# Kernel tuning notes

Measured on AMD Instinct MI355X. Metric: run time of the kernel, lower is better.

The kernel has to match this reference:

```python
import jax, jax.numpy as jnp
import numpy as np

D_MODEL = 1024
N_HEADS = 16
DEPTH = D_MODEL // N_HEADS


def setup_inputs() -> dict:
    key = jax.random.key(0)
    ks = jax.random.split(key, 11)
    B, S = 2, 2048
    s = 1.0 / np.sqrt(D_MODEL)
    return {
        "query": jax.random.normal(ks[0], (B, S, D_MODEL), jnp.float32),
        "key": jax.random.normal(ks[1], (B, S, D_MODEL), jnp.float32),
        "value": jax.random.normal(ks[2], (B, S, D_MODEL), jnp.float32),
        "Wq": jax.random.normal(ks[3], (D_MODEL, D_MODEL), jnp.float32) * s,
        "bq": jnp.zeros((D_MODEL,), jnp.float32),
        "Wk": jax.random.normal(ks[4], (D_MODEL, D_MODEL), jnp.float32) * s,
        "bk": jnp.zeros((D_MODEL,), jnp.float32),
        "Wv": jax.random.normal(ks[5], (D_MODEL, D_MODEL), jnp.float32) * s,
        "bv": jnp.zeros((D_MODEL,), jnp.float32),
        "Wo": jax.random.normal(ks[6], (D_MODEL, D_MODEL), jnp.float32) * s,
        "bo": jnp.zeros((D_MODEL,), jnp.float32),
    }


def _split_heads(x):
    B, S, _ = x.shape
    return x.reshape(B, S, N_HEADS, DEPTH).transpose(0, 2, 1, 3)  # [B,H,S,depth]


def reference(query, key, value, Wq, bq, Wk, bk, Wv, bv, Wo, bo):
    q = _split_heads(query @ Wq.T + bq)   # [B,H,S,d]
    k = _split_heads(key @ Wk.T + bk)
    v = _split_heads(value @ Wv.T + bv)
    scale = 1.0 / jnp.sqrt(jnp.asarray(DEPTH, jnp.float32))
    scores = jnp.einsum('bhqd,bhkd->bhqk', q, k) * scale  # [B,H,S,S]
    attn = jax.nn.softmax(scores, axis=-1)
    ctx = jnp.einsum('bhqk,bhkd->bhqd', attn, v)          # [B,H,S,d]
    B, H, S, d = ctx.shape
    ctx = ctx.transpose(0, 2, 1, 3).reshape(B, S, D_MODEL)
    out = ctx @ Wo.T + bo
    return out, attn
```

## Files before the change

### kernel.cpp

```cpp
#include <hip/hip_runtime.h>
#include <stdint.h>


#define DEV __device__ __forceinline__

typedef __attribute__((ext_vector_type(8))) short short8;
typedef __attribute__((ext_vector_type(4))) short short4v;
typedef __attribute__((ext_vector_type(4))) float f32x4;
typedef __attribute__((ext_vector_type(4))) uint32_t u32x4;

DEV short f2bf(float f) {
  uint32_t u = __builtin_bit_cast(uint32_t, f);
  u += 0x7fffu + ((u >> 16) & 1u);
  return (short)(u >> 16);
}

DEV uint32_t cvtpk_bf16(float a, float b) {
  uint32_t r;
  asm("v_cvt_pk_bf16_f32 %0, %1, %2" : "=v"(r) : "v"(a), "v"(b));
  return r;
}

DEV void gload_lds16(const void* g, void* l) {
  __builtin_amdgcn_global_load_lds(
      (const __attribute__((address_space(1))) void*)g,
      (__attribute__((address_space(3))) void*)l,
      16, 0, 0);
}

__global__ __launch_bounds__(256) void attn_fused(
    const short* __restrict__ q, const short* __restrict__ k,
    const short* __restrict__ vT, float* __restrict__ attn,
    short* __restrict__ ctx) {
  __shared__ __align__(16) char Ps[4 * 32 * 128];

  const int tid = threadIdx.x;
  const int lane = tid & 63;
  const int wm = tid >> 6;
  const int c = lane & 15;
  const int g = lane >> 4;
  const int orig = blockIdx.x;
  const int sid = (orig & 7) * 64 + (orig >> 3);
  const int qb = sid & 15;
  const int z = sid >> 4;

  const short* qz = q + (size_t)z * 131072 + (size_t)(qb * 128 + wm * 32) * 64;
  const short* kz = k + (size_t)z * 131072;
  const short* vz = vT + (size_t)z * 131072;
  float* az = attn + (size_t)z * 4194304 + (size_t)(qb * 128 + wm * 32) * 2048;

  short8 qf[2][2];
#pragma unroll
  for (int m = 0; m < 2; ++m)
#pragma unroll
    for (int kk = 0; kk < 2; ++kk)
      qf[m][kk] = *(const short8*)(qz + (m * 16 + c) * 64 + kk * 32 + g * 8);

  float l_part[2][4];
#pragma unroll
  for (int m = 0; m < 2; ++m)
#pragma unroll
    for (int j = 0; j < 4; ++j) l_part[m][j] = 0.f;

  for (int kt = 0; kt < 16; ++kt) {
    const short* kzt = kz + kt * 8192;
    f32x4 s[2][8];
#pragma unroll
    for (int m = 0; m < 2; ++m)
#pragma unroll
      for (int n = 0; n < 8; ++n) s[m][n] = f32x4{0.f, 0.f, 0.f, 0.f};
#pragma unroll
    for (int kk = 0; kk < 2; ++kk) {
#pragma unroll
      for (int n = 0; n < 8; ++n) {
        const short8 bf =
            *(const short8*)(kzt + (n * 16 + c) * 64 + kk * 32 + g * 8);
        s[0][n] = __builtin_amdgcn_mfma_f32_16x16x32_bf16(qf[0][kk], bf,
                                                          s[0][n], 0, 0, 0);
        s[1][n] = __builtin_amdgcn_mfma_f32_16x16x32_bf16(qf[1][kk], bf,
                                                          s[1][n], 0, 0, 0);
      }
    }
#pragma unroll
    for (int m = 0; m < 2; ++m)
#pragma unroll
      for (int j = 0; j < 4; ++j)
#pragma unroll
        for (int n = 0; n < 8; ++n) l_part[m][j] += __expf(s[m][n][j]);
  }

  float inv_l[2][4];
#pragma unroll
  for (int m = 0; m < 2; ++m)
#pragma unroll
    for (int j = 0; j < 4; ++j) {
      float l = l_part[m][j];
      l += __shfl_xor(l, 1, 64);
      l += __shfl_xor(l, 2, 64);
      l += __shfl_xor(l, 4, 64);
      l += __shfl_xor(l, 8, 64);
      inv_l[m][j] = 1.0f / l;
    }

  f32x4 o[2][4];
#pragma unroll
  for (int m = 0; m < 2; ++m)
#pragma unroll
    for (int n = 0; n < 4; ++n) o[m][n] = f32x4{0.f, 0.f, 0.f, 0.f};

  char* Pw = Ps + wm * 4096;

  for (int kt = 0; kt < 16; ++kt) {
    const short* kzt = kz + kt * 8192;
    f32x4 s[2][8];
#pragma unroll
    for (int m = 0; m < 2; ++m)
#pragma unroll
      for (int n = 0; n < 8; ++n) s[m][n] = f32x4{0.f, 0.f, 0.f, 0.f};
#pragma unroll
    for (int kk = 0; kk < 2; ++kk) {
#pragma unroll
      for (int n = 0; n < 8; ++n) {
        const short8 bf =
            *(const short8*)(kzt + (n * 16 + c) * 64 + kk * 32 + g * 8);
        s[0][n] = __builtin_amdgcn_mfma_f32_16x16x32_bf16(qf[0][kk], bf,
                                                          s[0][n], 0, 0, 0);
        s[1][n] = __builtin_amdgcn_mfma_f32_16x16x32_bf16(qf[1][kk], bf,
                                                          s[1][n], 0, 0, 0);
      }
    }
#pragma unroll
    for (int m = 0; m < 2; ++m)
#pragma unroll
      for (int j = 0; j < 4; ++j) {
        const float il = inv_l[m][j];
#pragma unroll
        for (int n = 0; n < 8; ++n) s[m][n][j] = __expf(s[m][n][j]) * il;
      }
#pragma unroll
    for (int m = 0; m < 2; ++m)
#pragma unroll
      for (int n = 0; n < 8; ++n)
#pragma unroll
        for (int j = 0; j < 4; ++j)
          __builtin_nontemporal_store(
              s[m][n][j], az + (size_t)(m * 16 + g * 4 + j) * 2048 +
                              kt * 128 + n * 16 + c);
#pragma unroll
    for (int kc = 0; kc < 4; ++kc) {
#pragma unroll
      for (int m = 0; m < 2; ++m)
#pragma unroll
        for (int nn = 0; nn < 2; ++nn)
#pragma unroll
          for (int j = 0; j < 4; ++j) {
            const int r = m * 16 + g * 4 + j;
            *(float*)(Pw + r * 128 +
                      (((nn * 16 + c) * 4) ^ ((r & 7) << 4))) =
                s[m][kc * 2 + nn][j];
          }
      short8 paf[2];
#pragma unroll
      for (int m = 0; m < 2; ++m) {
        const int r = m * 16 + c;
        const int X = (r & 7) << 4;
        const f32x4 lo = *(const f32x4*)(Pw + r * 128 + ((g * 32) ^ X));
        const f32x4 hi = *(const f32x4*)(Pw + r * 128 + ((g * 32 + 16) ^ X));
        u32x4 pk;
        pk[0] = cvtpk_bf16(lo[0], lo[1]);
        pk[1] = cvtpk_bf16(lo[2], lo[3]);
        pk[2] = cvtpk_bf16(hi[0], hi[1]);
        pk[3] = cvtpk_bf16(hi[2], hi[3]);
        paf[m] = __builtin_bit_cast(short8, pk);
      }
#pragma unroll
      for (int n2 = 0; n2 < 4; ++n2) {
        const short8 vf = *(const short8*)(vz + (size_t)(n2 * 16 + c) * 2048 +
                                           kt * 128 + kc * 32 + g * 8);
        o[0][n2] = __builtin_amdgcn_mfma_f32_16x16x32_bf16(paf[0], vf,
                                                           o[0][n2], 0, 0, 0);
        o[1][n2] = __builtin_amdgcn_mfma_f32_16x16x32_bf16(paf[1], vf,
                                                           o[1][n2], 0, 0, 0);
      }
    }
  }

  const int b = z >> 4, h = z & 15;
#pragma unroll
  for (int m = 0; m < 2; ++m)
#pragma unroll
    for (int n2 = 0; n2 < 4; ++n2)
#pragma unroll
      for (int j = 0; j < 4; ++j)
        ctx[((size_t)(b * 2048 + qb * 128 + wm * 32 + m * 16 + g * 4 + j)) *
                1024 + h * 64 + n2 * 16 + c] = f2bf(o[m][n2][j]);
}

enum { M_PROJ = 0, M_OUT = 3 };

struct GP {
  const void* A0; const void* A1; const void* A2;
  const short* B;
  const float* b0; const float* b1; const float* b2;
  void* C;
  int lda, ldb, K;
  long aBS, bBS;
};

template<int WM, int WN, int AM, int AN, bool CONVA, int MODE>
__global__ __launch_bounds__(256) void gemm_nt(GP p) {
  constexpr int BM = WM * 16 * AM;
  constexpr int BN = WN * 16 * AN;
  static_assert(WM * WN == 4, "4 waves / 256 threads");
  __shared__ __align__(16) char As[BM * 128];
  __shared__ __align__(16) char Bs[BN * 128];

  const int tid = threadIdx.x;
  const int lane = tid & 63;
  const int z = blockIdx.y;
  const int orig = blockIdx.x;
  const int sid = (orig & 7) * 32 + (orig >> 3);
  const int bm0 = (sid >> 3) * BM;
  const int bn0 = (sid & 7) * BN;

  const void* Aroot; const float* bias;
  if constexpr (MODE == M_PROJ) {
    if constexpr (CONVA)
      Aroot = (z == 0) ? p.A0 : (z == 1 ? p.A1 : p.A2);
    else
      Aroot = p.A0;
    bias = (z == 0) ? p.b0 : (z == 1 ? p.b1 : p.b2);
  } else {
    Aroot = p.A0; bias = p.b0;
  }

  f32x4 acc[AM][AN];
#pragma unroll
  for (int m = 0; m < AM; ++m)
#pragma unroll
    for (int n = 0; n < AN; ++n) acc[m][n] = f32x4{0.f, 0.f, 0.f, 0.f};

  const int wave = tid >> 6;
  const int wm = wave / WN;
  const int wn = wave % WN;

  const int nK = p.K >> 6;
  for (int kt = 0; kt < nK; ++kt) {
    if constexpr (CONVA) {
      const float* Af = (const float*)Aroot + (size_t)z * p.aBS +
                        (size_t)bm0 * p.lda + kt * 64;
#pragma unroll
      for (int sw = 0; sw < BM / 16; ++sw) {
        const int r = sw * 16 + (tid >> 4);
        const int s8 = tid & 15;
        const float4 v = *(const float4*)(Af + (size_t)r * p.lda + s8 * 4);
        short4v oo;
        oo[0] = f2bf(v.x); oo[1] = f2bf(v.y); oo[2] = f2bf(v.z); oo[3] = f2bf(v.w);
        const int boff = (r * 128 + s8 * 8) ^ ((r & 7) << 4);
        *(short4v*)(As + boff) = oo;
      }
    } else {
      const short* Ab = (const short*)Aroot + (size_t)z * p.aBS +
                        (size_t)bm0 * p.lda + kt * 64;
#pragma unroll
      for (int sw = 0; sw < BM / 32; ++sw) {
        const int r = sw * 32 + (tid >> 3);
        const int c8 = (tid & 7) ^ (r & 7);
        gload_lds16(Ab + (size_t)r * p.lda + c8 * 8, As + (sw * 256 + tid) * 16);
      }
    }
    {
      const short* Bb = p.B + (size_t)z * p.bBS + (size_t)bn0 * p.ldb + kt * 64;
#pragma unroll
      for (int sw = 0; sw < BN / 32; ++sw) {
        const int r = sw * 32 + (tid >> 3);
        const int c8 = (tid & 7) ^ (r & 7);
        gload_lds16(Bb + (size_t)r * p.ldb + c8 * 8, Bs + (sw * 256 + tid) * 16);
      }
    }
    __syncthreads();
#pragma unroll
    for (int kk = 0; kk < 2; ++kk) {
      const int kb = kk * 64 + (lane >> 4) * 16;
      short8 aF[AM], bF[AN];
#pragma unroll
      for (int m = 0; m < AM; ++m) {
        const int r = wm * (16 * AM) + m * 16 + (lane & 15);
        aF[m] = *(const short8*)(As + ((r * 128 + kb) ^ ((r & 7) << 4)));
      }
#pragma unroll
      for (int n = 0; n < AN; ++n) {
        const int r = wn * (16 * AN) + n * 16 + (lane & 15);
        bF[n] = *(const short8*)(Bs + ((r * 128 + kb) ^ ((r & 7) << 4)));
      }
#pragma unroll
      for (int m = 0; m < AM; ++m)
#pragma unroll
        for (int n = 0; n < AN; ++n)
          acc[m][n] = __builtin_amdgcn_mfma_f32_16x16x32_bf16(
              aF[m], bF[n], acc[m][n], 0, 0, 0);
    }
    __syncthreads();
  }

#pragma unroll
  for (int m = 0; m < AM; ++m) {
#pragma unroll
    for (int n = 0; n < AN; ++n) {
#pragma unroll
      for (int j = 0; j < 4; ++j) {
        const int gm = bm0 + wm * (16 * AM) + m * 16 + ((lane >> 4) << 2) + j;
        const int gn = bn0 + wn * (16 * AN) + n * 16 + (lane & 15);
        const float v = acc[m][n][j];
        if constexpr (MODE == M_PROJ) {
          float vb = v + bias[gn];
          if (z == 0) vb *= 0.125f;
          const int b = gm >> 11, s = gm & 2047;
          const int h = gn >> 6, d = gn & 63;
          short* C = (short*)p.C;
          if (z < 2) {
            C[(size_t)z * 4194304 + (((size_t)(b * 16 + h) * 2048 + s) * 64 + d)] = f2bf(vb);
          } else {
            C[(size_t)2 * 4194304 + (((size_t)(b * 16 + h) * 64 + d) * 2048 + s)] = f2bf(vb);
          }
        } else {
          __builtin_nontemporal_store(
              v + bias[gn], (float*)p.C + (size_t)gm * 1024 + gn);
        }
      }
    }
  }
}

__global__ __launch_bounds__(256) void cvt_all(
    const float* q, const float* k, const float* v, const float* w0,
    const float* w1, const float* w2, const float* w3, short* xb, short* Wb) {
  const int y = blockIdx.y;
  const float* src; short* dst; int n;
  if (y < 3) {
    src = (y == 0) ? q : (y == 1) ? k : v;
    dst = xb + (size_t)y * 4194304; n = 4194304;
  } else {
    src = (y == 3) ? w0 : (y == 4) ? w1 : (y == 5) ? w2 : w3;
    dst = Wb + (size_t)(y - 3) * 1048576; n = 1048576;
  }
  const int i = (blockIdx.x * 256 + threadIdx.x) * 4;
  if (i >= n) return;
  const float4 val = *(const float4*)(src + i);
  short4v s;
  s[0] = f2bf(val.x); s[1] = f2bf(val.y); s[2] = f2bf(val.z); s[3] = f2bf(val.w);
  *(short4v*)(dst + i) = s;
}

__global__ __launch_bounds__(256) void cvt_w(const float* w0, const float* w1,
                                             const float* w2, const float* w3,
                                             short* out) {
  const float* w = (blockIdx.y == 0) ? w0 : (blockIdx.y == 1) ? w1
                 : (blockIdx.y == 2) ? w2 : w3;
  short* o = out + (size_t)blockIdx.y * 1048576;
  const int i = (blockIdx.x * 256 + threadIdx.x) * 4;
  const float4 v = *(const float4*)(w + i);
  short4v s;
  s[0] = f2bf(v.x); s[1] = f2bf(v.y); s[2] = f2bf(v.z); s[3] = f2bf(v.w);
  *(short4v*)(o + i) = s;
}

extern "C" void kernel_launch(void* const* d_in, const int* in_sizes, int n_in,
                              void* d_out, int out_size, void* d_ws, size_t ws_size,
                              hipStream_t stream) {
  const float* query = (const float*)d_in[0];
  const float* key_  = (const float*)d_in[1];
  const float* value = (const float*)d_in[2];
  const float* Wq = (const float*)d_in[3];
  const float* bq = (const float*)d_in[4];
  const float* Wk = (const float*)d_in[5];
  const float* bk = (const float*)d_in[6];
  const float* Wv = (const float*)d_in[7];
  const float* bv = (const float*)d_in[8];
  const float* Wo = (const float*)d_in[9];
  const float* bo = (const float*)d_in[10];

  float* out  = (float*)d_out;
  float* attn = (float*)d_out + 4194304;
  short* ws   = (short*)d_ws;

  const bool big_ws = ws_size >= (size_t)64 * 1024 * 1024;

  if (big_ws) {
    short* xb  = ws;
    short* Wb  = ws + 3 * 4194304;
    short* qkv = ws + 3 * 4194304 + 4 * 1048576;
    short* ctx = qkv + 3 * 4194304;

    cvt_all<<<dim3(4096, 7), 256, 0, stream>>>(query, key_, value, Wq, Wk, Wv,
                                               Wo, xb, Wb);
    {
      GP p{};
      p.A0 = xb;
      p.B = Wb; p.b0 = bq; p.b1 = bk; p.b2 = bv;
      p.C = qkv;
      p.lda = 1024; p.ldb = 1024; p.K = 1024;
      p.aBS = 4194304; p.bBS = 1048576;
      gemm_nt<2, 2, 4, 4, false, M_PROJ><<<dim3(256, 3), 256, 0, stream>>>(p);
    }
    attn_fused<<<dim3(512), 256, 0, stream>>>(
        qkv, qkv + 4194304, qkv + 2 * 4194304, attn, ctx);
    {
      GP p{};
      p.A0 = ctx;
      p.B = Wb + 3 * 1048576;
      p.b0 = bo;
      p.C = out;
      p.lda = 1024; p.ldb = 1024; p.K = 1024;
      p.aBS = 0; p.bBS = 0;
      gemm_nt<2, 2, 4, 4, false, M_OUT><<<dim3(256, 1), 256, 0, stream>>>(p);
    }
  } else {
    short* Wb  = ws;
    short* qkv = ws + 4194304;
    short* ctx = ws + 4 * 4194304;

    cvt_w<<<dim3(1024, 4), 256, 0, stream>>>(Wq, Wk, Wv, Wo, Wb);
    {
      GP p{};
      p.A0 = query; p.A1 = key_; p.A2 = value;
      p.B = Wb; p.b0 = bq; p.b1 = bk; p.b2 = bv;
      p.C = qkv;
      p.lda = 1024; p.ldb = 1024; p.K = 1024;
      p.aBS = 0; p.bBS = 1048576;
      gemm_nt<2, 2, 4, 4, true, M_PROJ><<<dim3(256, 3), 256, 0, stream>>>(p);
    }
    attn_fused<<<dim3(512), 256, 0, stream>>>(
        qkv, qkv + 4194304, qkv + 2 * 4194304, attn, ctx);
    {
      GP p{};
      p.A0 = ctx;
      p.B = Wb + 3 * 1048576;
      p.b0 = bo;
      p.C = out;
      p.lda = 1024; p.ldb = 1024; p.K = 1024;
      p.aBS = 0; p.bBS = 0;
      gemm_nt<2, 2, 4, 4, false, M_OUT><<<dim3(256, 1), 256, 0, stream>>>(p);
    }
  }
}
```

Measured before the change: 302.9 us.

## Compute transposed scores so P feeds PV MFMA via shuffles instead of LDS

The attention kernel now computes S^T (K as the A operand, Q as B), so each lane holds four consecutive key columns. This allows vectorized 16-byte nontemporal stores of the attention matrix and lets the bf16 P fragment for the PV MFMA be assembled with cross-lane shuffles instead of an LDS round trip. Each wave now handles 16 query rows instead of 32, the grid doubles to 1024 blocks, and launch bounds request 4 blocks per CU. The cost is that K fragments are reused by half as many rows, so K and V global loads per unit of work double.

```diff
diff --git a/kernel.cpp b/kernel.cpp
--- a/kernel.cpp
+++ b/kernel.cpp
@@ -28,172 +28,124 @@
       16, 0, 0);
 }
 
-__global__ __launch_bounds__(256) void attn_fused(
+__global__ __launch_bounds__(256, 4) void attn_fused(
     const short* __restrict__ q, const short* __restrict__ k,
     const short* __restrict__ vT, float* __restrict__ attn,
     short* __restrict__ ctx) {
-  __shared__ __align__(16) char Ps[4 * 32 * 128];
-
   const int tid = threadIdx.x;
   const int lane = tid & 63;
   const int wm = tid >> 6;
   const int c = lane & 15;
   const int g = lane >> 4;
+  const bool godd = (g & 1) != 0;
+  const bool ghi = g >= 2;
   const int orig = blockIdx.x;
-  const int sid = (orig & 7) * 64 + (orig >> 3);
-  const int qb = sid & 15;
-  const int z = sid >> 4;
-
-  const short* qz = q + (size_t)z * 131072 + (size_t)(qb * 128 + wm * 32) * 64;
+  const int sid = (orig & 7) * 128 + (orig >> 3);
+  const int qb = sid & 31;
+  const int z = sid >> 5;
+
+  const short* qz = q + (size_t)z * 131072 + (size_t)(qb * 64 + wm * 16) * 64;
   const short* kz = k + (size_t)z * 131072;
   const short* vz = vT + (size_t)z * 131072;
-  float* az = attn + (size_t)z * 4194304 + (size_t)(qb * 128 + wm * 32) * 2048;
-
-  short8 qf[2][2];
-#pragma unroll
-  for (int m = 0; m < 2; ++m)
-#pragma unroll
-    for (int kk = 0; kk < 2; ++kk)
-      qf[m][kk] = *(const short8*)(qz + (m * 16 + c) * 64 + kk * 32 + g * 8);
-
-  float l_part[2][4];
-#pragma unroll
-  for (int m = 0; m < 2; ++m)
-#pragma unroll
-    for (int j = 0; j < 4; ++j) l_part[m][j] = 0.f;
-
+  float* az = attn + (size_t)z * 4194304 + (size_t)(qb * 64 + wm * 16) * 2048;
+
+  short8 qf[2];
+  qf[0] = *(const short8*)(qz + c * 64 + g * 8);
+  qf[1] = *(const short8*)(qz + c * 64 + 32 + g * 8);
+
+  f32x4 lacc = f32x4{0.f, 0.f, 0.f, 0.f};
   for (int kt = 0; kt < 16; ++kt) {
     const short* kzt = kz + kt * 8192;
-    f32x4 s[2][8];
-#pragma unroll
-    for (int m = 0; m < 2; ++m)
-#pragma unroll
-      for (int n = 0; n < 8; ++n) s[m][n] = f32x4{0.f, 0.f, 0.f, 0.f};
-#pragma unroll
-    for (int kk = 0; kk < 2; ++kk) {
+    f32x4 s[8];
+#pragma unroll
+    for (int n = 0; n < 8; ++n) s[n] = f32x4{0.f, 0.f, 0.f, 0.f};
+#pragma unroll
+    for (int kk = 0; kk < 2; ++kk)
 #pragma unroll
       for (int n = 0; n < 8; ++n) {
-        const short8 bf =
+        const short8 kf =
             *(const short8*)(kzt + (n * 16 + c) * 64 + kk * 32 + g * 8);
-        s[0][n] = __builtin_amdgcn_mfma_f32_16x16x32_bf16(qf[0][kk], bf,
-                                                          s[0][n], 0, 0, 0);
-        s[1][n] = __builtin_amdgcn_mfma_f32_16x16x32_bf16(qf[1][kk], bf,
-                                                          s[1][n], 0, 0, 0);
-      }
-    }
-#pragma unroll
-    for (int m = 0; m < 2; ++m)
-#pragma unroll
-      for (int j = 0; j < 4; ++j)
-#pragma unroll
-        for (int n = 0; n < 8; ++n) l_part[m][j] += __expf(s[m][n][j]);
-  }
-
-  float inv_l[2][4];
-#pragma unroll
-  for (int m = 0; m < 2; ++m)
-#pragma unroll
-    for (int j = 0; j < 4; ++j) {
-      float l = l_part[m][j];
-      l += __shfl_xor(l, 1, 64);
-      l += __shfl_xor(l, 2, 64);
-      l += __shfl_xor(l, 4, 64);
-      l += __shfl_xor(l, 8, 64);
-      inv_l[m][j] = 1.0f / l;
-    }
-
-  f32x4 o[2][4];
-#pragma unroll
-  for (int m = 0; m < 2; ++m)
-#pragma unroll
-    for (int n = 0; n < 4; ++n) o[m][n] = f32x4{0.f, 0.f, 0.f, 0.f};
-
-  char* Pw = Ps + wm * 4096;
+        s[n] = __builtin_amdgcn_mfma_f32_16x16x32_bf16(kf, qf[kk], s[n], 0, 0, 0);
+      }
+#pragma unroll
+    for (int n = 0; n < 8; ++n) {
+      f32x4 e;
+#pragma unroll
+      for (int j = 0; j < 4; ++j) e[j] = __expf(s[n][j]);
+      lacc += e;
+    }
+  }
+  float l = lacc[0] + lacc[1] + lacc[2] + lacc[3];
+  l += __shfl_xor(l, 16, 64);
+  l += __shfl_xor(l, 32, 64);
+  const float il = 1.0f / l;
+
+  f32x4 o[4];
+#pragma unroll
+  for (int n2 = 0; n2 < 4; ++n2) o[n2] = f32x4{0.f, 0.f, 0.f, 0.f};
 
   for (int kt = 0; kt < 16; ++kt) {
     const short* kzt = kz + kt * 8192;
-    f32x4 s[2][8];
-#pragma unroll
-    for (int m = 0; m < 2; ++m)
-#pragma unroll
-      for (int n = 0; n < 8; ++n) s[m][n] = f32x4{0.f, 0.f, 0.f, 0.f};
-#pragma unroll
-    for (int kk = 0; kk < 2; ++kk) {
+    f32x4 s[8];
+#pragma unroll
+    for (int n = 0; n < 8; ++n) s[n] = f32x4{0.f, 0.f, 0.f, 0.f};
+#pragma unroll
+    for (int kk = 0; kk < 2; ++kk)
 #pragma unroll
       for (int n = 0; n < 8; ++n) {
-        const short8 bf =
+        const short8 kf =
             *(const short8*)(kzt + (n * 16 + c) * 64 + kk * 32 + g * 8);
-        s[0][n] = __builtin_amdgcn_mfma_f32_16x16x32_bf16(qf[0][kk], bf,
-                                                          s[0][n], 0, 0, 0);
-        s[1][n] = __builtin_amdgcn_mfma_f32_16x16x32_bf16(qf[1][kk], bf,
-                                                          s[1][n], 0, 0, 0);
-      }
-    }
-#pragma unroll
-    for (int m = 0; m < 2; ++m)
+        s[n] = __builtin_amdgcn_mfma_f32_16x16x32_bf16(kf, qf[kk], s[n], 0, 0, 0);
+      }
+    float* azt = az + (size_t)c * 2048 + kt * 128 + g * 4;
+#pragma unroll
+    for (int kc = 0; kc < 4; ++kc) {
+      const int n0 = 2 * kc, n1 = 2 * kc + 1;
 #pragma unroll
       for (int j = 0; j < 4; ++j) {
-        const float il = inv_l[m][j];
-#pragma unroll
-        for (int n = 0; n < 8; ++n) s[m][n][j] = __expf(s[m][n][j]) * il;
-      }
-#pragma unroll
-    for (int m = 0; m < 2; ++m)
-#pragma unroll
-      for (int n = 0; n < 8; ++n)
-#pragma unroll
-        for (int j = 0; j < 4; ++j)
-          __builtin_nontemporal_store(
-              s[m][n][j], az + (size_t)(m * 16 + g * 4 + j) * 2048 +
-                              kt * 128 + n * 16 + c);
-#pragma unroll
-    for (int kc = 0; kc < 4; ++kc) {
-#pragma unroll
-      for (int m = 0; m < 2; ++m)
-#pragma unroll
-        for (int nn = 0; nn < 2; ++nn)
-#pragma unroll
-          for (int j = 0; j < 4; ++j) {
-            const int r = m * 16 + g * 4 + j;
-            *(float*)(Pw + r * 128 +
-                      (((nn * 16 + c) * 4) ^ ((r & 7) << 4))) =
-                s[m][kc * 2 + nn][j];
-          }
-      short8 paf[2];
-#pragma unroll
-      for (int m = 0; m < 2; ++m) {
-        const int r = m * 16 + c;
-        const int X = (r & 7) << 4;
-        const f32x4 lo = *(const f32x4*)(Pw + r * 128 + ((g * 32) ^ X));
-        const f32x4 hi = *(const f32x4*)(Pw + r * 128 + ((g * 32 + 16) ^ X));
-        u32x4 pk;
-        pk[0] = cvtpk_bf16(lo[0], lo[1]);
-        pk[1] = cvtpk_bf16(lo[2], lo[3]);
-        pk[2] = cvtpk_bf16(hi[0], hi[1]);
-        pk[3] = cvtpk_bf16(hi[2], hi[3]);
-        paf[m] = __builtin_bit_cast(short8, pk);
-      }
+        s[n0][j] = __expf(s[n0][j]) * il;
+        s[n1][j] = __expf(s[n1][j]) * il;
+      }
+      __builtin_nontemporal_store(s[n0], (f32x4*)(azt + n0 * 16));
+      __builtin_nontemporal_store(s[n1], (f32x4*)(azt + n1 * 16));
+      const uint32_t x00 = cvtpk_bf16(s[n0][0], s[n0][1]);
+      const uint32_t x01 = cvtpk_bf16(s[n0][2], s[n0][3]);
+      const uint32_t x10 = cvtpk_bf16(s[n1][0], s[n1][1]);
+      const uint32_t x11 = cvtpk_bf16(s[n1][2], s[n1][3]);
+      const uint32_t cs0 = ghi ? x00 : x10;
+      const uint32_t cs1 = ghi ? x01 : x11;
+      const uint32_t cr0 = __shfl_xor(cs0, 32, 64);
+      const uint32_t cr1 = __shfl_xor(cs1, 32, 64);
+      const uint32_t lw0 = ghi ? cr0 : x00;
+      const uint32_t lw1 = ghi ? cr1 : x01;
+      const uint32_t hw0 = ghi ? x10 : cr0;
+      const uint32_t hw1 = ghi ? x11 : cr1;
+      const uint32_t ns0 = godd ? lw0 : hw0;
+      const uint32_t ns1 = godd ? lw1 : hw1;
+      const uint32_t nr0 = __shfl_xor(ns0, 16, 64);
+      const uint32_t nr1 = __shfl_xor(ns1, 16, 64);
+      u32x4 fr;
+      fr[0] = godd ? nr0 : lw0;
+      fr[1] = godd ? nr1 : lw1;
+      fr[2] = godd ? hw0 : nr0;
+      fr[3] = godd ? hw1 : nr1;
+      const short8 paf = __builtin_bit_cast(short8, fr);
 #pragma unroll
       for (int n2 = 0; n2 < 4; ++n2) {
         const short8 vf = *(const short8*)(vz + (size_t)(n2 * 16 + c) * 2048 +
                                            kt * 128 + kc * 32 + g * 8);
-        o[0][n2] = __builtin_amdgcn_mfma_f32_16x16x32_bf16(paf[0], vf,
-                                                           o[0][n2], 0, 0, 0);
-        o[1][n2] = __builtin_amdgcn_mfma_f32_16x16x32_bf16(paf[1], vf,
-                                                           o[1][n2], 0, 0, 0);
+        o[n2] = __builtin_amdgcn_mfma_f32_16x16x32_bf16(paf, vf, o[n2], 0, 0, 0);
       }
     }
   }
 
   const int b = z >> 4, h = z & 15;
 #pragma unroll
-  for (int m = 0; m < 2; ++m)
-#pragma unroll
-    for (int n2 = 0; n2 < 4; ++n2)
-#pragma unroll
-      for (int j = 0; j < 4; ++j)
-        ctx[((size_t)(b * 2048 + qb * 128 + wm * 32 + m * 16 + g * 4 + j)) *
-                1024 + h * 64 + n2 * 16 + c] = f2bf(o[m][n2][j]);
+  for (int n2 = 0; n2 < 4; ++n2)
+#pragma unroll
+    for (int j = 0; j < 4; ++j)
+      ctx[((size_t)(b * 2048 + qb * 64 + wm * 16 + g * 4 + j)) * 1024 +
+          h * 64 + n2 * 16 + c] = f2bf(o[n2][j]);
 }
 
 enum { M_PROJ = 0, M_OUT = 3 };
@@ -403,7 +355,7 @@
       p.aBS = 4194304; p.bBS = 1048576;
       gemm_nt<2, 2, 4, 4, false, M_PROJ><<<dim3(256, 3), 256, 0, stream>>>(p);
     }
-    attn_fused<<<dim3(512), 256, 0, stream>>>(
+    attn_fused<<<dim3(1024), 256, 0, stream>>>(
         qkv, qkv + 4194304, qkv + 2 * 4194304, attn, ctx);
     {
       GP p{};
@@ -430,7 +382,7 @@
       p.aBS = 0; p.bBS = 1048576;
       gemm_nt<2, 2, 4, 4, true, M_PROJ><<<dim3(256, 3), 256, 0, stream>>>(p);
     }
-    attn_fused<<<dim3(512), 256, 0, stream>>>(
+    attn_fused<<<dim3(1024), 256, 0, stream>>>(
         qkv, qkv + 4194304, qkv + 2 * 4194304, attn, ctx);
     {
       GP p{};
```

Result: slower. 443.3 us (+46.4%).
